# Kernel optimization log

Measured on AMD Instinct MI355X. Metric: run time of the kernel, lower is better.

## Reference

```python
import jax, jax.numpy as jnp
import numpy as np

BINS = 10


def setup_inputs() -> dict:
    key = jax.random.key(0)
    k1, k2 = jax.random.split(key)
    N = 16777216
    x = jax.random.normal(k1, (N, 1), dtype=jnp.float32)
    target = jax.random.randint(k2, (N,), 0, 2, dtype=jnp.int32)
    return {"x": x, "target": target}


def reference(x, target):
    # GHMC_Loss forward (binary, num_classes=1), first call (_last_bin_count is None).
    N = x.shape[0]
    logits = x[:, 0]                                   # [N]
    t = target.astype(x.dtype)                         # [N]

    # gradient norm g = |sigmoid(x) - t|  (detached in original)
    g = jnp.abs(jax.nn.sigmoid(logits) - t)            # [N]
    bin_idx = jnp.clip(
        jnp.floor(g * (BINS - 0.0001)).astype(jnp.int32), 0, BINS - 1
    )                                                  # [N]

    # single-pass histogram via scatter-add
    bin_count = jnp.zeros((BINS,), x.dtype).at[bin_idx].add(1.0)
    nonempty = (bin_count > 0).sum().astype(x.dtype)
    gd = jnp.maximum(bin_count * nonempty, 1e-6)
    beta = jnp.asarray(N, x.dtype) / gd                # [BINS]
    weights = beta[bin_idx]                            # [N] gather

    # stable BCE with logits: logaddexp(0, x) - x*t
    ce = jnp.logaddexp(jnp.zeros_like(logits), logits) - logits * t
    return jnp.mean(ce * weights)
```

## Files before the change

### kernel.cpp

```cpp
#include <hip/hip_runtime.h>

#define BINS 10
#define TPB 256
#define MAX_BLOCKS 2048
#define NTHR 9

__device__ __constant__ const float c_thr[NTHR] = {
    -2.1972135f, -1.3862819f, -0.8472836f, -0.4054484f, 2.00002e-5f,
     0.4054901f,  0.8473312f,  1.3863444f,  2.1973246f
};

__device__ __forceinline__ void ghmc_accum(float z, int t, float* A, float* C) {
    unsigned ub = __float_as_uint(z) ^ ((unsigned)t << 31);
    float u  = __uint_as_float(ub);
    float e  = __expf(-fabsf(u));
    float q  = 1.0f + e;
    float ce = fmaxf(u, 0.0f) + __logf(q);
    A[0] += ce;
    #pragma unroll
    for (int k = 1; k <= NTHR; ++k) {
        float m = (u >= c_thr[k - 1]) ? 1.0f : 0.0f;
        A[k]    = fmaf(m, ce, A[k]);
        C[k - 1] += m;
    }
}

__global__ __launch_bounds__(TPB) void ghmc_main(const float* __restrict__ x,
                                                 const int* __restrict__ tgt,
                                                 float* __restrict__ partial,
                                                 int nvec, int ntotal) {
    float A[BINS];
    float C[NTHR];
    #pragma unroll
    for (int b = 0; b < BINS; ++b) A[b] = 0.0f;
    #pragma unroll
    for (int k = 0; k < NTHR; ++k) C[k] = 0.0f;

    const float4* __restrict__ x4 = (const float4*)x;
    const int4*  __restrict__ t4 = (const int4*)tgt;
    const int tid = threadIdx.x;
    const int stride = gridDim.x * TPB;

    #pragma unroll 2
    for (int gi = blockIdx.x * TPB + tid; gi < nvec; gi += stride) {
        float4 xv = x4[gi];
        int4   tv = t4[gi];
        ghmc_accum(xv.x, tv.x, A, C);
        ghmc_accum(xv.y, tv.y, A, C);
        ghmc_accum(xv.z, tv.z, A, C);
        ghmc_accum(xv.w, tv.w, A, C);
    }
    if (blockIdx.x == 0) {
        for (int i = nvec * 4 + tid; i < ntotal; i += TPB)
            ghmc_accum(x[i], tgt[i], A, C);
    }

    #pragma unroll
    for (int b = 0; b < BINS; ++b) {
        #pragma unroll
        for (int o = 32; o > 0; o >>= 1) A[b] += __shfl_down(A[b], o);
    }
    #pragma unroll
    for (int k = 0; k < NTHR; ++k) {
        #pragma unroll
        for (int o = 32; o > 0; o >>= 1) C[k] += __shfl_down(C[k], o);
    }
    __shared__ float red[TPB / 64][2 * BINS];
    const int wid = tid >> 6, lane = tid & 63;
    if (lane == 0) {
        #pragma unroll
        for (int b = 0; b < BINS; ++b) red[wid][b] = A[b];
        #pragma unroll
        for (int k = 0; k < NTHR; ++k) red[wid][BINS + k] = C[k];
    }
    __syncthreads();
    if (tid < BINS + NTHR) {
        float v = 0.0f;
        #pragma unroll
        for (int w = 0; w < TPB / 64; ++w) v += red[w][tid];
        partial[blockIdx.x * (2 * BINS) + tid] = v;
    }
}

__global__ __launch_bounds__(TPB) void ghmc_final(const float* __restrict__ partial,
                                                  float* __restrict__ out,
                                                  int nblocks, int ntotal) {
    float acc[2 * BINS];
    #pragma unroll
    for (int k = 0; k < 2 * BINS; ++k) acc[k] = 0.0f;
    for (int row = threadIdx.x; row < nblocks; row += TPB) {
        const float* p = partial + row * (2 * BINS);
        #pragma unroll
        for (int k = 0; k < 2 * BINS; ++k) acc[k] += p[k];
    }
    #pragma unroll
    for (int k = 0; k < 2 * BINS; ++k) {
        #pragma unroll
        for (int o = 32; o > 0; o >>= 1) acc[k] += __shfl_down(acc[k], o);
    }
    __shared__ float red[TPB / 64][2 * BINS];
    const int wid = threadIdx.x >> 6, lane = threadIdx.x & 63;
    if (lane == 0) {
        #pragma unroll
        for (int k = 0; k < 2 * BINS; ++k) red[wid][k] = acc[k];
    }
    __syncthreads();
    if (threadIdx.x == 0) {
        float A[BINS + 1], C[BINS + 1];
        #pragma unroll
        for (int b = 0; b < BINS; ++b) {
            float v = 0.0f;
            #pragma unroll
            for (int w = 0; w < TPB / 64; ++w) v += red[w][b];
            A[b] = v;
        }
        A[BINS] = 0.0f;
        C[0] = (float)ntotal;
        #pragma unroll
        for (int k = 1; k <= NTHR; ++k) {
            float v = 0.0f;
            #pragma unroll
            for (int w = 0; w < TPB / 64; ++w) v += red[w][BINS + k - 1];
            C[k] = v;
        }
        C[BINS] = 0.0f;
        float ne = 0.0f;
        #pragma unroll
        for (int b = 0; b < BINS; ++b) {
            float c = C[b] - C[b + 1];
            ne += (c > 0.0f) ? 1.0f : 0.0f;
        }
        float res = 0.0f;
        #pragma unroll
        for (int b = 0; b < BINS; ++b) {
            float s = A[b] - A[b + 1];
            float c = C[b] - C[b + 1];
            res += s / fmaxf(c * ne, 1e-6f);
        }
        out[0] = res;
    }
}

extern "C" void kernel_launch(void* const* d_in, const int* in_sizes, int n_in,
                              void* d_out, int out_size, void* d_ws, size_t ws_size,
                              hipStream_t stream) {
    const float* x   = (const float*)d_in[0];
    const int*   tgt = (const int*)d_in[1];
    float* out     = (float*)d_out;
    float* partial = (float*)d_ws;

    int N    = in_sizes[0];
    int nvec = N / 4;

    int blocks = MAX_BLOCKS;
    int maxrows = (int)(ws_size / (2 * BINS * sizeof(float)));
    if (blocks > maxrows) blocks = maxrows;
    int need = (nvec + TPB - 1) / TPB;
    if (blocks > need) blocks = need;
    if (blocks < 1) blocks = 1;

    ghmc_main<<<blocks, TPB, 0, stream>>>(x, tgt, partial, nvec, N);
    ghmc_final<<<1, TPB, 0, stream>>>(partial, out, blocks, N);
}
```

Baseline: 152.5 us.

## Software-pipeline global loads with inline asm and explicit vmcnt waits

Replaces the grid-stride loop with a 4-deep register pipeline. Raw global_load_dwordx4 instructions are issued through inline asm, and explicit s_waitcnt vmcnt values keep several loads in flight while earlier data is computed. Launch bounds also request 4 waves per SIMD. The intent is to hide memory latency in a bandwidth-bound reduction, at the cost of more registers and fragile hand-managed wait counts that bypass compiler scheduling.

```diff
diff --git a/kernel.cpp b/kernel.cpp
--- a/kernel.cpp
+++ b/kernel.cpp
@@ -4,6 +4,10 @@
 #define TPB 256
 #define MAX_BLOCKS 2048
 #define NTHR 9
+#define DEPTH 4
+
+typedef float f32x4 __attribute__((ext_vector_type(4)));
+typedef int   i32x4 __attribute__((ext_vector_type(4)));
 
 __device__ __constant__ const float c_thr[NTHR] = {
     -2.1972135f, -1.3862819f, -0.8472836f, -0.4054484f, 2.00002e-5f,
@@ -25,10 +29,32 @@
     }
 }
 
-__global__ __launch_bounds__(TPB) void ghmc_main(const float* __restrict__ x,
-                                                 const int* __restrict__ tgt,
-                                                 float* __restrict__ partial,
-                                                 int nvec, int ntotal) {
+#define ISSUE(xs, ts, idx) do {                                   \
+    const f32x4* _xa = x4 + (idx);                                \
+    const i32x4* _ta = t4 + (idx);                                \
+    asm volatile("global_load_dwordx4 %0, %2, off\n\t"            \
+                 "global_load_dwordx4 %1, %3, off"                \
+                 : "=&v"(xs), "=&v"(ts)                           \
+                 : "v"(_xa), "v"(_ta)                             \
+                 : "memory");                                     \
+} while (0)
+
+#define COMPUTE(xs, ts) do {                                      \
+    ghmc_accum((xs).x, (ts).x, A, C);                             \
+    ghmc_accum((xs).y, (ts).y, A, C);                             \
+    ghmc_accum((xs).z, (ts).z, A, C);                             \
+    ghmc_accum((xs).w, (ts).w, A, C);                             \
+} while (0)
+
+#define WAITV(n) do {                                             \
+    asm volatile("s_waitcnt vmcnt(" #n ")" ::: "memory");         \
+    __builtin_amdgcn_sched_barrier(0);                            \
+} while (0)
+
+__global__ __launch_bounds__(TPB, 4) void ghmc_main(const float* __restrict__ x,
+                                                    const int* __restrict__ tgt,
+                                                    float* __restrict__ partial,
+                                                    int nvec, int ntotal) {
     float A[BINS];
     float C[NTHR];
     #pragma unroll
@@ -36,19 +62,48 @@
     #pragma unroll
     for (int k = 0; k < NTHR; ++k) C[k] = 0.0f;
 
-    const float4* __restrict__ x4 = (const float4*)x;
-    const int4*  __restrict__ t4 = (const int4*)tgt;
+    const f32x4* __restrict__ x4 = (const f32x4*)x;
+    const i32x4* __restrict__ t4 = (const i32x4*)tgt;
     const int tid = threadIdx.x;
     const int stride = gridDim.x * TPB;
-
-    #pragma unroll 2
-    for (int gi = blockIdx.x * TPB + tid; gi < nvec; gi += stride) {
-        float4 xv = x4[gi];
-        int4   tv = t4[gi];
-        ghmc_accum(xv.x, tv.x, A, C);
-        ghmc_accum(xv.y, tv.y, A, C);
-        ghmc_accum(xv.z, tv.z, A, C);
-        ghmc_accum(xv.w, tv.w, A, C);
+    const int nfull  = nvec / stride;
+    const int gi0 = blockIdx.x * TPB + tid;
+    int it_done = 0;
+
+    if (nfull >= DEPTH) {
+        f32x4 xs0, xs1, xs2, xs3;
+        i32x4 ts0, ts1, ts2, ts3;
+        int gp = gi0;
+        ISSUE(xs0, ts0, gp); gp += stride;
+        ISSUE(xs1, ts1, gp); gp += stride;
+        ISSUE(xs2, ts2, gp); gp += stride;
+        ISSUE(xs3, ts3, gp); gp += stride;
+        const int nchunk = nfull / DEPTH;
+        for (int c = 0; c < nchunk - 1; ++c) {
+            WAITV(6); COMPUTE(xs0, ts0); ISSUE(xs0, ts0, gp); gp += stride;
+            WAITV(6); COMPUTE(xs1, ts1); ISSUE(xs1, ts1, gp); gp += stride;
+            WAITV(6); COMPUTE(xs2, ts2); ISSUE(xs2, ts2, gp); gp += stride;
+            WAITV(6); COMPUTE(xs3, ts3); ISSUE(xs3, ts3, gp); gp += stride;
+        }
+        WAITV(6); COMPUTE(xs0, ts0);
+        WAITV(4); COMPUTE(xs1, ts1);
+        WAITV(2); COMPUTE(xs2, ts2);
+        WAITV(0); COMPUTE(xs3, ts3);
+        it_done = nchunk * DEPTH;
+    }
+    for (int it = it_done; it < nfull; ++it) {
+        int g = gi0 + it * stride;
+        f32x4 xv = x4[g];
+        i32x4 tv = t4[g];
+        COMPUTE(xv, tv);
+    }
+    {
+        int gr = gi0 + nfull * stride;
+        if (gr < nvec) {
+            f32x4 xv = x4[gr];
+            i32x4 tv = t4[gr];
+            COMPUTE(xv, tv);
+        }
     }
     if (blockIdx.x == 0) {
         for (int i = nvec * 4 + tid; i < ntotal; i += TPB)
```

Result: no change. 152.8 us (+0.2%).

## Double-buffer input tiles via global_load_lds async loads with vmcnt waits

Applied to the files above, without the earlier changes.

Replaces the grid-stride register-load loop with a per-wave double-buffered pipeline. It issues direct global-to-LDS loads for the next tile while computing the current one, and synchronises with explicit s_waitcnt vmcnt waits. The grid is halved to 1024 blocks and launch bounds now request occupancy. The goal is to hide memory latency in this bandwidth-bound reduction. In exchange it adds LDS usage and a fragile hand-coded wait count, and each wave reads only its own LDS slice, so no barrier is needed.

```diff
diff --git a/kernel.cpp b/kernel.cpp
--- a/kernel.cpp
+++ b/kernel.cpp
@@ -2,8 +2,16 @@
 
 #define BINS 10
 #define TPB 256
-#define MAX_BLOCKS 2048
+#define NW (TPB / 64)
+#define MAX_BLOCKS 1024
 #define NTHR 9
+#define Q 2
+#define CALLS (2 * Q)
+
+typedef float f32x4 __attribute__((ext_vector_type(4)));
+typedef int   i32x4 __attribute__((ext_vector_type(4)));
+
+static_assert(CALLS == 4, "WAITV literals below assume 4 staging calls/tile");
 
 __device__ __constant__ const float c_thr[NTHR] = {
     -2.1972135f, -1.3862819f, -0.8472836f, -0.4054484f, 2.00002e-5f,
@@ -25,10 +33,15 @@
     }
 }
 
-__global__ __launch_bounds__(TPB) void ghmc_main(const float* __restrict__ x,
-                                                 const int* __restrict__ tgt,
-                                                 float* __restrict__ partial,
-                                                 int nvec, int ntotal) {
+#define WAITV(n) do {                                             \
+    asm volatile("s_waitcnt vmcnt(" #n ")" ::: "memory");         \
+    __builtin_amdgcn_sched_barrier(0);                            \
+} while (0)
+
+__global__ __launch_bounds__(TPB, 4) void ghmc_main(const float* __restrict__ x,
+                                                    const int* __restrict__ tgt,
+                                                    float* __restrict__ partial,
+                                                    int nvec, int ntotal) {
     float A[BINS];
     float C[NTHR];
     #pragma unroll
@@ -36,15 +49,62 @@
     #pragma unroll
     for (int k = 0; k < NTHR; ++k) C[k] = 0.0f;
 
-    const float4* __restrict__ x4 = (const float4*)x;
-    const int4*  __restrict__ t4 = (const int4*)tgt;
-    const int tid = threadIdx.x;
-    const int stride = gridDim.x * TPB;
-
-    #pragma unroll 2
-    for (int gi = blockIdx.x * TPB + tid; gi < nvec; gi += stride) {
-        float4 xv = x4[gi];
-        int4   tv = t4[gi];
+    const f32x4* __restrict__ x4 = (const f32x4*)x;
+    const i32x4* __restrict__ t4 = (const i32x4*)tgt;
+    const int tid  = threadIdx.x;
+    const int wid  = tid >> 6;
+    const int lane = tid & 63;
+
+    __shared__ f32x4 ldsx[2][NW][Q][64];
+    __shared__ i32x4 ldst[2][NW][Q][64];
+
+    const int GPB    = TPB * Q;
+    const int ntiles = nvec / (GPB * gridDim.x);
+    const int covered = ntiles * GPB * gridDim.x;
+
+    #define STAGE(b, tb) do {                                                  \
+        int _g = (tb) + wid * (Q * 64) + lane;                                 \
+        _Pragma("unroll")                                                      \
+        for (int _j = 0; _j < Q; ++_j) {                                       \
+            __builtin_amdgcn_global_load_lds(                                  \
+                (const __attribute__((address_space(1))) void*)(x4 + _g + _j * 64), \
+                (__attribute__((address_space(3))) void*)&ldsx[b][wid][_j][0], \
+                16, 0, 0);                                                     \
+            __builtin_amdgcn_global_load_lds(                                  \
+                (const __attribute__((address_space(1))) void*)(t4 + _g + _j * 64), \
+                (__attribute__((address_space(3))) void*)&ldst[b][wid][_j][0], \
+                16, 0, 0);                                                     \
+        }                                                                      \
+    } while (0)
+
+    #define CTILE(b) do {                                                      \
+        _Pragma("unroll")                                                      \
+        for (int _j = 0; _j < Q; ++_j) {                                       \
+            f32x4 xv = ldsx[b][wid][_j][lane];                                 \
+            i32x4 tv = ldst[b][wid][_j][lane];                                 \
+            ghmc_accum(xv.x, tv.x, A, C);                                      \
+            ghmc_accum(xv.y, tv.y, A, C);                                      \
+            ghmc_accum(xv.z, tv.z, A, C);                                      \
+            ghmc_accum(xv.w, tv.w, A, C);                                      \
+        }                                                                      \
+    } while (0)
+
+    if (ntiles > 0) {
+        STAGE(0, (0 * gridDim.x + blockIdx.x) * GPB);
+        for (int t = 0; t < ntiles; ++t) {
+            int cur = t & 1;
+            if (t + 1 < ntiles) {
+                STAGE(cur ^ 1, ((t + 1) * gridDim.x + blockIdx.x) * GPB);
+                WAITV(4);
+            } else {
+                WAITV(0);
+            }
+            CTILE(cur);
+        }
+    }
+    for (int g = covered + blockIdx.x * TPB + tid; g < nvec; g += gridDim.x * TPB) {
+        f32x4 xv = x4[g];
+        i32x4 tv = t4[g];
         ghmc_accum(xv.x, tv.x, A, C);
         ghmc_accum(xv.y, tv.y, A, C);
         ghmc_accum(xv.z, tv.z, A, C);
@@ -65,8 +125,7 @@
         #pragma unroll
         for (int o = 32; o > 0; o >>= 1) C[k] += __shfl_down(C[k], o);
     }
-    __shared__ float red[TPB / 64][2 * BINS];
-    const int wid = tid >> 6, lane = tid & 63;
+    __shared__ float red[NW][2 * BINS];
     if (lane == 0) {
         #pragma unroll
         for (int b = 0; b < BINS; ++b) red[wid][b] = A[b];
@@ -77,7 +136,7 @@
     if (tid < BINS + NTHR) {
         float v = 0.0f;
         #pragma unroll
-        for (int w = 0; w < TPB / 64; ++w) v += red[w][tid];
+        for (int w = 0; w < NW; ++w) v += red[w][tid];
         partial[blockIdx.x * (2 * BINS) + tid] = v;
     }
 }
```

After: 152.6 us. About the same (+0.0%).
